# Kernel tuning notes

Hardware: AMD Instinct MI355X
Metric: run time of the kernel (lower is better)

## Reference

```python
import jax, jax.numpy as jnp
import numpy as np

SLEN, BSZ, D_MODEL, N_HEAD, D_HEAD, PROJ_DIM = 2048, 2, 1024, 16, 64, 256
LN_EPS = 1e-5
PRIME_EPS = 1e-4


def setup_inputs() -> dict:
    key = jax.random.key(0)
    ks = jax.random.split(key, 4)
    h = jax.random.normal(ks[0], (SLEN, BSZ, D_MODEL), jnp.float32)
    W_qkvb = jax.random.normal(ks[1], (D_MODEL, N_HEAD * (3 * D_HEAD + 1)), jnp.float32) * (D_MODEL ** -0.5)
    W_o = jax.random.normal(ks[2], (N_HEAD * D_HEAD, D_MODEL), jnp.float32) * ((N_HEAD * D_HEAD) ** -0.5)
    ln_gamma = jnp.ones((D_MODEL,), jnp.float32)
    ln_beta = jnp.zeros((D_MODEL,), jnp.float32)
    # orthogonal random matrix (d_head, proj_dim): blocks of orthonormal cols, rows scaled to norm sqrt(d)
    rng = np.random.default_rng(0)
    blocks = []
    for _ in range(PROJ_DIM // D_HEAD):
        qm, _ = np.linalg.qr(rng.standard_normal((D_HEAD, D_HEAD)))
        blocks.append(qm)
    pm = np.concatenate(blocks, axis=1) * np.sqrt(D_HEAD)
    proj_matrix = jnp.asarray(pm, jnp.float32)  # (d_head, proj_dim)
    return {"h": h, "W_qkvb": W_qkvb, "W_o": W_o, "ln_gamma": ln_gamma,
            "ln_beta": ln_beta, "proj_matrix": proj_matrix}


def prime(x, pm):
    # FAVOR+ hyperbolic softmax-kernel features. x: (B,H,L,d), pm: (d,m) -> (B,H,L,2m)
    d = x.shape[-1]
    m = pm.shape[-1]
    xn = x * (d ** -0.25)
    proj = jnp.einsum('bhld,dm->bhlm', xn, pm)
    hnorm = 0.5 * jnp.sum(xn * xn, axis=-1, keepdims=True)
    feat = jnp.concatenate([jnp.exp(proj - hnorm), jnp.exp(-proj - hnorm)], axis=-1)
    return ((2 * m) ** -0.5) * (feat + PRIME_EPS)


def layer_norm(x, gamma, beta):
    mu = jnp.mean(x, axis=-1, keepdims=True)
    var = jnp.mean(jnp.square(x - mu), axis=-1, keepdims=True)
    return (x - mu) * jax.lax.rsqrt(var + LN_EPS) * gamma + beta


def reference(h, W_qkvb, W_o, ln_gamma, ln_beta, proj_matrix):
    slen, bsz, _ = h.shape
    qkvb = (h @ W_qkvb).reshape(slen, bsz, N_HEAD, 3 * D_HEAD + 1)
    q, k, v, hb = jnp.split(qkvb, [D_HEAD, 2 * D_HEAD, 3 * D_HEAD], axis=-1)
    hb = jax.nn.sigmoid(hb)
    # (L,B,H,*) -> (B,H,L,*)
    q = q.transpose(1, 2, 0, 3)
    k = k.transpose(1, 2, 0, 3)
    v = v.transpose(1, 2, 0, 3)
    hb = hb.transpose(1, 2, 0, 3)
    qp = prime(q, proj_matrix)
    kp = prime(k, proj_matrix)
    kp = kp / kp.sum(-1, keepdims=True)
    qp = qp / qp.sum(-1, keepdims=True)
    # time-major for the scan: (L,B,H,*)
    qpT = qp.transpose(2, 0, 1, 3)
    kpT = kp.transpose(2, 0, 1, 3)
    vT = v.transpose(2, 0, 1, 3)
    hbT = hb.transpose(2, 0, 1, 3)
    W0 = jnp.zeros((bsz, N_HEAD, 2 * PROJ_DIM, D_HEAD), h.dtype)

    def step(W, inp):
        qt, kt, vt, bt = inp  # (B,H,2m),(B,H,2m),(B,H,d),(B,H,1)
        v_old = jnp.einsum('bhpd,bhp->bhd', W, kt)
        W = W + jnp.einsum('bhp,bhd->bhpd', kt, bt * (vt - v_old))
        out = jnp.einsum('bhpd,bhp->bhd', W, qt)
        return W, out

    _, outs = jax.lax.scan(step, W0, (qpT, kpT, vT, hbT))  # outs: (L,B,H,d)
    scale = D_HEAD ** -0.5
    layer_out = (scale * outs).reshape(slen, bsz, N_HEAD * D_HEAD)
    attn_out = layer_out @ W_o
    return layer_norm(h + attn_out, ln_gamma, ln_beta)
```

## Files before the change

### kernel.cpp

```cpp
#include <hip/hip_runtime.h>
#include <hip/hip_bf16.h>

#define LSEQ   2048
#define BSZN   2
#define DMODEL 1024
#define NHEAD  16
#define DH     64
#define MPROJ  256
#define PF     512
#define CHK    64
#define NCHK   32
#define BHN    32
#define NQKV   3088
#define NQPAD  3200

typedef __hip_bfloat16 bf16;
typedef short bf16x8 __attribute__((ext_vector_type(8)));
typedef float f32x4 __attribute__((ext_vector_type(4)));

#define MFMA(a, b, c) __builtin_amdgcn_mfma_f32_16x16x32_bf16(a, b, c, 0, 0, 0)

#define UNP(u, a, b) { a = __uint_as_float((unsigned)(u) << 16); b = __uint_as_float((unsigned)(u) & 0xffff0000u); }

static __device__ __forceinline__ float b2f(bf16 x) {
  unsigned short us = *(unsigned short*)&x;
  return __uint_as_float((unsigned)us << 16);
}
static __device__ __forceinline__ bf16 f2b(float x) { return __float2bfloat16(x); }
static __device__ __forceinline__ unsigned pkbf(float a, float b) {
  bf16 x = __float2bfloat16(a), y = __float2bfloat16(b);
  return ((unsigned)(*(unsigned short*)&y) << 16) | (unsigned)(*(unsigned short*)&x);
}

static __device__ __forceinline__ void gl_lds16(const void* gsrc, void* ldst) {
  __builtin_amdgcn_global_load_lds(
      (const __attribute__((address_space(1))) unsigned int*)gsrc,
      (__attribute__((address_space(3))) unsigned int*)ldst, 16, 0, 0);
}

#define MEMFENCE asm volatile("" ::: "memory")
#define WAITV(n) asm volatile("s_waitcnt vmcnt(" #n ")" ::: "memory")
#define WAITLGKM asm volatile("s_waitcnt lgkmcnt(0)" ::: "memory")
#define BARRIER() __builtin_amdgcn_s_barrier()

__global__ __launch_bounds__(256)
void k_cvth(const float* __restrict__ h, bf16* __restrict__ hbf)
{
  const int gt = blockIdx.x * 256 + threadIdx.x;
  const int r = gt >> 7, ug = gt & 127;
  const int grp = ug >> 3, u = ug & 7;
  const float4 f0 = *(const float4*)&h[(size_t)r * 1024 + grp * 64 + u * 8];
  const float4 f1 = *(const float4*)&h[(size_t)r * 1024 + grp * 64 + u * 8 + 4];
  uint4 o;
  o.x = pkbf(f0.x, f0.y); o.y = pkbf(f0.z, f0.w);
  o.z = pkbf(f1.x, f1.y); o.w = pkbf(f1.z, f1.w);
  *(uint4*)&hbf[(size_t)r * 1024 + grp * 64 + ((u ^ (r & 7)) << 3)] = o;
}

__global__ __launch_bounds__(256)
void k_cvtw(const float* __restrict__ W, bf16* __restrict__ WT, int nsrc)
{
  __shared__ float sT[64][65];
  const int tid = threadIdx.x;
  const int n0 = blockIdx.x * 64, k0 = blockIdx.y * 64;
#pragma unroll
  for (int j = 0; j < 16; j++) {
    const int e = j * 256 + tid;
    const int r = e >> 6, c = e & 63;
    sT[r][c] = (n0 + c < nsrc) ? W[(size_t)(k0 + r) * nsrc + n0 + c] : 0.f;
  }
  __syncthreads();
#pragma unroll
  for (int j = 0; j < 2; j++) {
    const int uid = j * 256 + tid;
    const int rp = uid >> 3, u = uid & 7;
    uint4 o;
    o.x = pkbf(sT[u * 8 + 0][rp], sT[u * 8 + 1][rp]);
    o.y = pkbf(sT[u * 8 + 2][rp], sT[u * 8 + 3][rp]);
    o.z = pkbf(sT[u * 8 + 4][rp], sT[u * 8 + 5][rp]);
    o.w = pkbf(sT[u * 8 + 6][rp], sT[u * 8 + 7][rp]);
    *(uint4*)&WT[(size_t)(n0 + rp) * 1024 + k0 + ((u ^ (rp & 7)) << 3)] = o;
  }
}

__global__ __launch_bounds__(256)
void k_cvtpm(const float* __restrict__ pm, bf16* __restrict__ pmThi,
             bf16* __restrict__ pmTlo)
{
  const int n = threadIdx.x;
  float v[64];
#pragma unroll
  for (int d = 0; d < 64; d++) v[d] = pm[d * MPROJ + n] * 0.35355339059327373f;
  const int key = n & 7;
#pragma unroll
  for (int u = 0; u < 8; u++) {
    unsigned hi[4], lo[4];
#pragma unroll
    for (int j = 0; j < 4; j++) {
      const float a = v[u * 8 + j * 2], b = v[u * 8 + j * 2 + 1];
      const bf16 ah = f2b(a), bh_ = f2b(b);
      const float ar = a - b2f(ah), br = b - b2f(bh_);
      hi[j] = ((unsigned)(*(const unsigned short*)&bh_) << 16) | (unsigned)(*(const unsigned short*)&ah);
      const bf16 al = f2b(ar), bl = f2b(br);
      lo[j] = ((unsigned)(*(const unsigned short*)&bl) << 16) | (unsigned)(*(const unsigned short*)&al);
    }
    *(uint4*)&pmThi[(size_t)n * 64 + ((u ^ key) << 3)] = make_uint4(hi[0], hi[1], hi[2], hi[3]);
    *(uint4*)&pmTlo[(size_t)n * 64 + ((u ^ key) << 3)] = make_uint4(lo[0], lo[1], lo[2], lo[3]);
  }
}

#define GEMM_STAGE(Abase, Bbase, kt, b) {                                      \
  const size_t kb = (size_t)(kt) * 128;           \
  _Pragma("unroll")                                                            \
  for (int j = 0; j < 4; j++) {                                                \
    const int row = (w * 4 + j) * 8 + (lane >> 3);                             \
    gl_lds16((const char*)(Abase) + (size_t)(m0 + row) * 2048 + kb + (lane & 7) * 16, \
             &sA[b][(w * 4 + j) * 1024]);                                      \
  }                                                                            \
  _Pragma("unroll")                                                            \
  for (int j = 0; j < 4; j++) {                                                \
    const int row = (w * 4 + j) * 8 + (lane >> 3);                             \
    gl_lds16((const char*)(Bbase) + (size_t)(n0 + row) * 2048 + kb + (lane & 7) * 16, \
             &sB[b][(w * 4 + j) * 1024]);                                      \
  } }

#define GEMM_COMPUTE(b) {                                                      \
  _Pragma("unroll")                                                            \
  for (int ks = 0; ks < 2; ks++) {                                             \
    bf16x8 af[4], bfr[4];                                                      \
    _Pragma("unroll")                                                          \
    for (int f = 0; f < 4; f++) {                                              \
      const int row = wm * 64 + f * 16 + l16;                                  \
      af[f] = *(const bf16x8*)&sA[b][row * 128 + (((ks * 4 + lg) ^ xs) << 4)]; \
    }                                                                          \
    _Pragma("unroll")                                                          \
    for (int f = 0; f < 4; f++) {                                              \
      const int row = wn * 64 + f * 16 + l16;                                  \
      bfr[f] = *(const bf16x8*)&sB[b][row * 128 + (((ks * 4 + lg) ^ xs) << 4)]; \
    }                                                                          \
    _Pragma("unroll")                                                          \
    for (int fm = 0; fm < 4; fm++)                                             \
      _Pragma("unroll")                                                        \
      for (int fn = 0; fn < 4; fn++)                                           \
        acc[fm][fn] = MFMA(af[fm], bfr[fn], acc[fm][fn]);                      \
  } }

#define GEMM_PREAMBLE                                                          \
  __shared__ __align__(16) char sA[2][16384];                                  \
  __shared__ __align__(16) char sB[2][16384];                                  \
  const int tid = threadIdx.x, w = tid >> 6, lane = tid & 63;                  \
  const int l16 = lane & 15, lg = lane >> 4;                                   \
  const int wm = w >> 1, wn = w & 1;                                           \
  const int m0 = blockIdx.y * 128, n0 = blockIdx.x * 128;                      \
  const int xs = l16 & 7;                                                      \
  f32x4 acc[4][4];                                                             \
  _Pragma("unroll")                                                            \
  for (int i = 0; i < 4; i++)                                                  \
    _Pragma("unroll")                                                          \
    for (int j = 0; j < 4; j++) acc[i][j] = (f32x4){0.f, 0.f, 0.f, 0.f};

__global__ __launch_bounds__(256, 2)
void k_gemm_qkvb(const bf16* __restrict__ A, const bf16* __restrict__ B,
                 bf16* __restrict__ qh, bf16* __restrict__ kh,
                 bf16* __restrict__ vh, float* __restrict__ bbuf)
{
  GEMM_PREAMBLE
  GEMM_STAGE(A, B, 0, 0);
  __syncthreads();
  for (int kt = 0; kt < 16; kt++) {
    const int b = kt & 1;
    if (kt < 15) GEMM_STAGE(A, B, kt + 1, b ^ 1);
    GEMM_COMPUTE(b);
    __syncthreads();
  }
#pragma unroll
  for (int fm = 0; fm < 4; fm++)
#pragma unroll
    for (int fn = 0; fn < 4; fn++)
#pragma unroll
      for (int reg = 0; reg < 4; reg++) {
        const int m = m0 + wm * 64 + fm * 16 + lg * 4 + reg;
        const int n = n0 + wn * 64 + fn * 16 + l16;
        if (n >= NQKV) continue;
        const float v = acc[fm][fn][reg];
        const int l = m >> 1, bidx = m & 1;
        const int hd = n / 193;
        const int rem = n - hd * 193;
        const int bhi = bidx * NHEAD + hd;
        const size_t o = ((size_t)bhi * LSEQ + l) * DH;
        if (rem < 64) {
          const int d = rem;
          qh[o + ((((d >> 3) ^ (l & 7)) << 3) | (d & 7))] = f2b(v);
        } else if (rem < 128) {
          const int d = rem - 64;
          kh[o + ((((d >> 3) ^ (l & 7)) << 3) | (d & 7))] = f2b(v);
        } else if (rem < 192) {
          vh[o + rem - 128] = f2b(v);
        } else {
          bbuf[(size_t)bhi * LSEQ + l] = 1.f / (1.f + __expf(-v));
        }
      }
}

__global__ __launch_bounds__(256, 2)
void k_gemm_out(const bf16* __restrict__ A, const bf16* __restrict__ B,
                const float* __restrict__ h, float* __restrict__ ao)
{
  GEMM_PREAMBLE
  GEMM_STAGE(A, B, 0, 0);
  __syncthreads();
  for (int kt = 0; kt < 16; kt++) {
    const int b = kt & 1;
    if (kt < 15) GEMM_STAGE(A, B, kt + 1, b ^ 1);
    GEMM_COMPUTE(b);
    __syncthreads();
  }
#pragma unroll
  for (int fm = 0; fm < 4; fm++)
#pragma unroll
    for (int fn = 0; fn < 4; fn++)
#pragma unroll
      for (int reg = 0; reg < 4; reg++) {
        const int m = m0 + wm * 64 + fm * 16 + lg * 4 + reg;
        const int n = n0 + wn * 64 + fn * 16 + l16;
        const size_t o = (size_t)m * DMODEL + n;
        ao[o] = acc[fm][fn][reg] + h[o];
      }
}

__global__ __launch_bounds__(256, 2)
void k_featm(const bf16* __restrict__ qh, const bf16* __restrict__ kh,
             const bf16* __restrict__ pmThi, const bf16* __restrict__ pmTlo,
             bf16* __restrict__ Qp, bf16* __restrict__ Kp)
{
  __shared__ __align__(16) char sPM[2][32768];
  __shared__ __align__(16) char sX[8192];

  const int tid = threadIdx.x, w = tid >> 6, lane = tid & 63;
  const int l16 = lane & 15, lg = lane >> 4;
  const int xs = l16 & 7;
  const int l0 = blockIdx.x * 64, bhi = blockIdx.y;

#pragma unroll
  for (int j = 0; j < 8; j++)
    gl_lds16((const char*)pmThi + (size_t)(w * 8 + j) * 1024 + lane * 16,
             &sPM[0][(w * 8 + j) * 1024]);
#pragma unroll
  for (int j = 0; j < 8; j++)
    gl_lds16((const char*)pmTlo + (size_t)(w * 8 + j) * 1024 + lane * 16,
             &sPM[1][(w * 8 + j) * 1024]);
  {
    const char* qb = (const char*)(qh + ((size_t)bhi * LSEQ + l0) * DH);
#pragma unroll
    for (int j = 0; j < 2; j++)
      gl_lds16(qb + (size_t)(w * 2 + j) * 1024 + lane * 16, &sX[(w * 2 + j) * 1024]);
  }
  MEMFENCE;
  WAITV(0); BARRIER();

  const int srow = w * 16 + l16;
  const size_t gsr = (size_t)bhi * LSEQ + l0 + srow;

  for (int wh = 0; wh < 2; wh++) {
    bf16* dst = wh ? Kp : Qp;

    float hn;
    {
      const char* xrow = &sX[srow * 128];
      const uint4 a0 = *(const uint4*)&xrow[lg * 32];
      const uint4 a1 = *(const uint4*)&xrow[lg * 32 + 16];
      float f0, f1, f2, f3, f4, f5, f6, f7, a = 0.f;
      UNP(a0.x, f0, f1); UNP(a0.y, f2, f3); UNP(a0.z, f4, f5); UNP(a0.w, f6, f7);
      a = fmaf(f0, f0, a); a = fmaf(f1, f1, a); a = fmaf(f2, f2, a); a = fmaf(f3, f3, a);
      a = fmaf(f4, f4, a); a = fmaf(f5, f5, a); a = fmaf(f6, f6, a); a = fmaf(f7, f7, a);
      UNP(a1.x, f0, f1); UNP(a1.y, f2, f3); UNP(a1.z, f4, f5); UNP(a1.w, f6, f7);
      a = fmaf(f0, f0, a); a = fmaf(f1, f1, a); a = fmaf(f2, f2, a); a = fmaf(f3, f3, a);
      a = fmaf(f4, f4, a); a = fmaf(f5, f5, a); a = fmaf(f6, f6, a); a = fmaf(f7, f7, a);
      a += __shfl_xor(a, 16); a += __shfl_xor(a, 32);
      hn = a * 0.0625f;
    }

    f32x4 acc[16];
#pragma unroll
    for (int i = 0; i < 16; i++) acc[i] = (f32x4){0.f, 0.f, 0.f, 0.f};
#pragma unroll
    for (int ks = 0; ks < 2; ks++) {
      const bf16x8 bx = *(const bf16x8*)&sX[srow * 128 + (((ks * 4 + lg) ^ xs) << 4)];
#pragma unroll
      for (int mt = 0; mt < 16; mt++) {
        const bf16x8 ah = *(const bf16x8*)&sPM[0][(mt * 16 + l16) * 128 + (((ks * 4 + lg) ^ xs) << 4)];
        acc[mt] = MFMA(ah, bx, acc[mt]);
        const bf16x8 al = *(const bf16x8*)&sPM[1][(mt * 16 + l16) * 128 + (((ks * 4 + lg) ^ xs) << 4)];
        acc[mt] = MFMA(al, bx, acc[mt]);
      }
    }

    if (wh == 0) {
      BARRIER();
      const char* kb = (const char*)(kh + ((size_t)bhi * LSEQ + l0) * DH);
#pragma unroll
      for (int j = 0; j < 2; j++)
        gl_lds16(kb + (size_t)(w * 2 + j) * 1024 + lane * 16, &sX[(w * 2 + j) * 1024]);
      MEMFENCE;
    }

    float ss = 0.f;
#pragma unroll
    for (int mt = 0; mt < 16; mt++)
#pragma unroll
      for (int r = 0; r < 4; r++) {
        const float p = acc[mt][r];
        ss += __expf(p - hn) + __expf(-p - hn);
      }
    ss += __shfl_xor(ss, 16); ss += __shfl_xor(ss, 32);
    const float D = ss + 0.0512f;
    const float cc = 1e-4f / D;
    const float eo = hn + __logf(D);

    const size_t gb = gsr * PF;
    const int half = (lg & 1) * 4;
    const int ub = lg >> 1;
#pragma unroll
    for (int mt = 0; mt < 16; mt++) {
      const float v0 = __expf(acc[mt][0] - eo) + cc;
      const float v1 = __expf(acc[mt][1] - eo) + cc;
      const float v2 = __expf(acc[mt][2] - eo) + cc;
      const float v3 = __expf(acc[mt][3] - eo) + cc;
      const float n0 = __expf(-acc[mt][0] - eo) + cc;
      const float n1 = __expf(-acc[mt][1] - eo) + cc;
      const float n2 = __expf(-acc[mt][2] - eo) + cc;
      const float n3 = __expf(-acc[mt][3] - eo) + cc;
      const int u = mt * 2 + ub;
      *(uint2*)&dst[gb + ((u ^ xs) << 3) + half] = make_uint2(pkbf(v0, v1), pkbf(v2, v3));
      *(uint2*)&dst[gb + (((u + 32) ^ xs) << 3) + half] = make_uint2(pkbf(n0, n1), pkbf(n2, n3));
      __builtin_amdgcn_sched_barrier(0);
    }

    if (wh == 0) { WAITV(32); BARRIER(); }
  }
}

__global__ __launch_bounds__(256, 2)
void k_sgsolve(const bf16* __restrict__ Kp, const bf16* __restrict__ Qp,
               const float* __restrict__ bbuf,
               bf16* __restrict__ Gl, bf16* __restrict__ Tm,
               bf16* __restrict__ KpT)
{
  __shared__ __align__(16) char bufK[2][8192];
  __shared__ __align__(16) char bufQ[2][8192];
  __shared__ float sS[CHK][65];
  __shared__ float sT[CHK][65];
  __shared__ float sBeta[CHK];

  const int tid = threadIdx.x, w = tid >> 6, lane = tid & 63;
  const int l16 = lane & 15, lg = lane >> 4;
  const int xs = l16 & 7;
  const int c = blockIdx.x, bhi = blockIdx.y;
  const size_t cb = ((size_t)bhi * LSEQ + (size_t)c * CHK) * PF;
  const size_t rowb = (size_t)bhi * LSEQ + (size_t)c * CHK;
  const size_t ktb = (((size_t)bhi * NCHK + c) * 512) * 64;
  const size_t sb = (((size_t)bhi * NCHK + c) * CHK) * CHK;

  if (tid < CHK) sBeta[tid] = bbuf[rowb + tid];

  f32x4 accS[4], accG[4];
#pragma unroll
  for (int i = 0; i < 4; i++) { accS[i] = (f32x4){0.f,0.f,0.f,0.f}; accG[i] = (f32x4){0.f,0.f,0.f,0.f}; }

#define SG_STAGE(win, b) {                                                     \
  _Pragma("unroll")                                                            \
  for (int j = 0; j < 2; j++) {                                                \
    const int row = w * 16 + j * 8 + (lane >> 3);                              \
    gl_lds16((const char*)(Kp + cb) + (size_t)row * 1024 + (size_t)(win) * 128 + (lane & 7) * 16, \
             &bufK[b][(w * 16 + j * 8) * 128]);                                \
  }                                                                            \
  _Pragma("unroll")                                                            \
  for (int j = 0; j < 2; j++) {                                                \
    const int row = w * 16 + j * 8 + (lane >> 3);                              \
    gl_lds16((const char*)(Qp + cb) + (size_t)row * 1024 + (size_t)(win) * 128 + (lane & 7) * 16, \
             &bufQ[b][(w * 16 + j * 8) * 128]);                                \
  } }

  SG_STAGE(0, 0);
  MEMFENCE;

  for (int win = 0; win < 8; win++) {
    const int b = win & 1;
    if (win < 7) { SG_STAGE(win + 1, b ^ 1); MEMFENCE; }
    if (win == 0)      { WAITV(4); }
    else if (win < 7)  { WAITV(6); }
    else               { WAITV(2); }
    BARRIER();

#pragma unroll
    for (int ks = 0; ks < 2; ks++) {
      const bf16x8 aK = *(const bf16x8*)&bufK[b][(16 * w + l16) * 128 + (((ks * 4 + lg) ^ xs) << 4)];
      const bf16x8 aQ = *(const bf16x8*)&bufQ[b][(16 * w + l16) * 128 + (((ks * 4 + lg) ^ xs) << 4)];
      bf16x8 bK[4];
#pragma unroll
      for (int nt = 0; nt < 4; nt++)
        bK[nt] = *(const bf16x8*)&bufK[b][(nt * 16 + l16) * 128 + (((ks * 4 + lg) ^ xs) << 4)];
#pragma unroll
      for (int nt = 0; nt < 4; nt++) {
        accS[nt] = MFMA(aK, bK[nt], accS[nt]);
        accG[nt] = MFMA(aQ, bK[nt], accG[nt]);
      }
    }

#pragma unroll
    for (int jj = 0; jj < 2; jj++) {
      const int idx = jj * 256 + tid;
      const int pl = idx >> 3, l8 = idx & 7;
      unsigned short v[8];
#pragma unroll
      for (int j = 0; j < 8; j++) {
        const int l = l8 * 8 + j;
        v[j] = *(const unsigned short*)&bufK[b][l * 128 + (((pl >> 3) ^ (l & 7)) << 4) + (pl & 7) * 2];
      }
      uint4 o;
      o.x = ((unsigned)v[1] << 16) | v[0];
      o.y = ((unsigned)v[3] << 16) | v[2];
      o.z = ((unsigned)v[5] << 16) | v[4];
      o.w = ((unsigned)v[7] << 16) | v[6];
      const int p = win * 64 + pl;
      *(uint4*)&KpT[ktb + (size_t)p * 64 + ((l8 ^ (p & 7)) << 3)] = o;
    }
    BARRIER();
  }
#undef SG_STAGE

#pragma unroll
  for (int nt = 0; nt < 4; nt++)
#pragma unroll
    for (int reg = 0; reg < 4; reg++) {
      const int ri = 16 * w + lg * 4 + reg;
      const int cj = nt * 16 + l16;
      sS[ri][cj] = accS[nt][reg];
      Gl[sb + ri * 64 + (((cj >> 3) ^ (ri & 7)) << 3) + (cj & 7)] =
          f2b((cj <= ri) ? accG[nt][reg] : 0.f);
    }
  __syncthreads();

  if (tid < CHK) {
    const int j = tid;
    for (int i = 0; i < CHK; i++) {
      float acc = (i == j) ? 1.f : 0.f;
      for (int k = 0; k < i; k++) acc = fmaf(-sS[i][k], sT[k][j], acc);
      sT[i][j] = sBeta[i] * acc;
    }
  }
  __syncthreads();
  for (int t = tid; t < CHK * CHK; t += 256) {
    const int r = t >> 6, ccj = t & 63;
    Tm[sb + r * 64 + (((ccj >> 3) ^ (r & 7)) << 3) + (ccj & 7)] = f2b(sT[r][ccj]);
  }
}

__global__ __launch_bounds__(512, 2)
void k_scan(const bf16* __restrict__ Kp, const bf16* __restrict__ Qp,
            const bf16* __restrict__ vh, const bf16* __restrict__ Tm,
            const bf16* __restrict__ Gl, const bf16* __restrict__ KpT,
            bf16* __restrict__ lobf)
{
  __shared__ __align__(16) char bufA[65536];
  __shared__ __align__(16) char bufB[65536];
  __shared__ __align__(16) char sWT[16384];
  __shared__ __align__(16) char suP[2048];
  __shared__ __align__(16) char sUT[2048];
  __shared__ __align__(16) float pbuf[4][16][16];

  const int tid = threadIdx.x;
  const int w = tid >> 6, lane = tid & 63;
  const int l16 = lane & 15, lg = lane >> 4;
  const int wp = w >> 1, h = w & 1;
  const int bhi = blockIdx.x & 31, dq = blockIdx.x >> 5;
  const int bidx = bhi >> 4, hd = bhi & 15;
  const int xs = l16 & 7;

  char* RA = bufA + w * 8192;
  char* RB = bufB + w * 8192;

  for (int i = tid; i < 4096; i += 512) ((unsigned*)sWT)[i] = 0u;

  f32x4 Wacc[4];
#pragma unroll
  for (int i = 0; i < 4; i++) Wacc[i] = (f32x4){0.f, 0.f, 0.f, 0.f};

  const size_t bh_base = (size_t)bhi * LSEQ * PF;
  const size_t tg0 = ((size_t)bhi * NCHK) * 4096;
  const size_t kt0 = ((size_t)bhi * NCHK) * (512 * 64);

  {
    const char* gt = (const char*)(KpT + kt0);
#pragma unroll
    for (int j = 0; j < 8; j++)
      gl_lds16(gt + (size_t)w * 8192 + j * 1024 + lane * 16, RB + j * 1024);
    const char* g = (const char*)(Kp + bh_base);
#pragma unroll
    for (int j = 0; j < 8; j++)
      gl_lds16(g + (size_t)(16 * wp + 2 * j + (lane >> 5)) * 1024 + h * 512 + (lane & 31) * 16,
               RA + j * 1024);
  }
  MEMFENCE;
  WAITV(0); WAITLGKM; BARRIER();

  for (int c = 0; c < NCHK; c++) {
    BARRIER();

    const size_t cb = bh_base + (size_t)c * CHK * PF;
    const bf16* TmC  = Tm + tg0 + (size_t)c * 4096;
    const bf16* GlC  = Gl + tg0 + (size_t)c * 4096;
    const char* QpC  = (const char*)(Qp + cb);
    const char* KpN  = (const char*)(Kp + cb + CHK * PF);
    const char* KpTN = (const char*)(KpT + kt0 + (size_t)(c + 1) * (512 * 64));
    const int trow = 16 * wp + l16;

    float v0 = 0.f, v1 = 0.f, v2 = 0.f, v3 = 0.f;
    bf16x8 tf0 = {}, tf1 = {}, gf0 = {}, gf1 = {};
    if (!h) {
      const bf16* vp = vh + ((size_t)bhi * LSEQ + c * 64 + wp * 16 + lg * 4) * 64 + dq * 16 + l16;
      v0 = b2f(vp[0]);   v1 = b2f(vp[64]);
      v2 = b2f(vp[128]); v3 = b2f(vp[192]);
      tf0 = *(const bf16x8*)&TmC[trow * 64 + ((lg ^ xs) << 3)];
      tf1 = *(const bf16x8*)&TmC[trow * 64 + (((4 + lg) ^ xs) << 3)];
      gf0 = *(const bf16x8*)&GlC[trow * 64 + ((lg ^ xs) << 3)];
      gf1 = *(const bf16x8*)&GlC[trow * 64 + (((4 + lg) ^ xs) << 3)];
    }
    MEMFENCE;
    if (!h) { WAITV(12); } else { WAITV(0); }

    f32x4 a0v = (f32x4){0.f,0.f,0.f,0.f}, a1v = (f32x4){0.f,0.f,0.f,0.f};
    bf16x8 wb[8];
#pragma unroll
    for (int ks = 0; ks < 8; ks += 2) {
      const bf16x8 aa0 = *(const bf16x8*)&RA[l16 * 512 + (((ks * 4 + lg) ^ xs) << 4)];
      wb[ks] = *(const bf16x8*)&sWT[l16 * 1024 + ((((h * 32 + ks * 4 + lg)) ^ xs) << 4)];
      a0v = MFMA(aa0, wb[ks], a0v);
      const bf16x8 aa1 = *(const bf16x8*)&RA[l16 * 512 + ((((ks + 1) * 4 + lg) ^ xs) << 4)];
      wb[ks + 1] = *(const bf16x8*)&sWT[l16 * 1024 + ((((h * 32 + (ks + 1) * 4 + lg)) ^ xs) << 4)];
      a1v = MFMA(aa1, wb[ks + 1], a1v);
    }
    if (h) {
      float4 pv;
      pv.x = a0v[0] + a1v[0]; pv.y = a0v[1] + a1v[1];
      pv.z = a0v[2] + a1v[2]; pv.w = a0v[3] + a1v[3];
      *(float4*)&pbuf[wp][l16][lg * 4] = pv;
    }
    WAITLGKM;
    BARRIER();

#pragma unroll
    for (int j = 0; j < 8; j++)
      gl_lds16(QpC + (size_t)(16 * wp + 2 * j + (lane >> 5)) * 1024 + h * 512 + (lane & 31) * 16,
               RA + j * 1024);
    MEMFENCE;

    if (!h) {
      WAITV(8);
      const float4 po = *(const float4*)&pbuf[wp][l16][lg * 4];
      const float u0 = v0 - (a0v[0] + a1v[0]) - po.x;
      const float u1 = v1 - (a0v[1] + a1v[1]) - po.y;
      const float u2 = v2 - (a0v[2] + a1v[2]) - po.z;
      const float u3 = v3 - (a0v[3] + a1v[3]) - po.w;
      const int l0r = 16 * wp + lg * 4;
      *(uint2*)&suP[l16 * 128 + (((l0r >> 3) ^ xs) << 4) + (l0r & 7) * 2] =
          make_uint2(pkbf(u0, u1), pkbf(u2, u3));
    }
    WAITLGKM;
    BARRIER();

    if (!h) {
      f32x4 ua = (f32x4){0.f,0.f,0.f,0.f};
      ua = MFMA(tf0, *(const bf16x8*)&suP[l16 * 128 + ((lg ^ xs) << 4)], ua);
      ua = MFMA(tf1, *(const bf16x8*)&suP[l16 * 128 + (((4 + lg) ^ xs) << 4)], ua);
      const int l0r = 16 * wp + lg * 4;
      *(uint2*)&sUT[l16 * 128 + (((l0r >> 3) ^ xs) << 4) + (l0r & 7) * 2] =
          make_uint2(pkbf(ua[0], ua[1]), pkbf(ua[2], ua[3]));
    }
    WAITLGKM;
    BARRIER();

    const bf16x8 bu0 = *(const bf16x8*)&sUT[l16 * 128 + ((lg ^ xs) << 4)];
    const bf16x8 bu1 = *(const bf16x8*)&sUT[l16 * 128 + (((4 + lg) ^ xs) << 4)];
#pragma unroll
    for (int mt = 0; mt < 4; mt++) {
      const int pr = mt * 16 + l16;
      const bf16x8 ka0 = *(const bf16x8*)&RB[pr * 128 + ((lg ^ xs) << 4)];
      Wacc[mt] = MFMA(ka0, bu0, Wacc[mt]);
      const bf16x8 ka1 = *(const bf16x8*)&RB[pr * 128 + (((4 + lg) ^ xs) << 4)];
      Wacc[mt] = MFMA(ka1, bu1, Wacc[mt]);
    }
    WAITLGKM;
    if (c < NCHK - 1) {
#pragma unroll
      for (int j = 0; j < 8; j++)
        gl_lds16(KpTN + (size_t)w * 8192 + j * 1024 + lane * 16, RB + j * 1024);
      MEMFENCE;
    }
#pragma unroll
    for (int mt = 0; mt < 4; mt++) {
      const int p0m = w * 64 + mt * 16 + lg * 4;
      *(uint2*)&sWT[l16 * 1024 + (((p0m >> 3) ^ xs) << 4) + (p0m & 7) * 2] =
          make_uint2(pkbf(Wacc[mt][0], Wacc[mt][1]), pkbf(Wacc[mt][2], Wacc[mt][3]));
    }

    if (c < NCHK - 1) { WAITV(8); } else { WAITV(0); }
    f32x4 o0 = (f32x4){0.f,0.f,0.f,0.f}, o1 = (f32x4){0.f,0.f,0.f,0.f};
#pragma unroll
    for (int ks = 0; ks < 8; ks += 2) {
      const bf16x8 qa0 = *(const bf16x8*)&RA[l16 * 512 + (((ks * 4 + lg) ^ xs) << 4)];
      o0 = MFMA(qa0, wb[ks], o0);
      const bf16x8 qa1 = *(const bf16x8*)&RA[l16 * 512 + ((((ks + 1) * 4 + lg) ^ xs) << 4)];
      o1 = MFMA(qa1, wb[ks + 1], o1);
    }
    WAITLGKM;
    if (c < NCHK - 1) {
#pragma unroll
      for (int j = 0; j < 8; j++)
        gl_lds16(KpN + (size_t)(16 * wp + 2 * j + (lane >> 5)) * 1024 + h * 512 + (lane & 31) * 16,
                 RA + j * 1024);
      MEMFENCE;
    }
    if (h) {
      float4 pv;
      pv.x = o0[0] + o1[0]; pv.y = o0[1] + o1[1];
      pv.z = o0[2] + o1[2]; pv.w = o0[3] + o1[3];
      *(float4*)&pbuf[wp][l16][lg * 4] = pv;
    } else {
      o0 = MFMA(gf0, bu0, o0);
      o1 = MFMA(gf1, bu1, o1);
    }
    WAITLGKM;
    BARRIER();

    if (!h) {
      const float4 po = *(const float4*)&pbuf[wp][l16][lg * 4];
      const float pr4[4] = {po.x, po.y, po.z, po.w};
      const int colb = hd * 64 + dq * 16 + l16;
#pragma unroll
      for (int reg = 0; reg < 4; reg++) {
        const int l = c * 64 + 16 * wp + lg * 4 + reg;
        const int r = l * BSZN + bidx;
        const int cp = (colb & ~63) | ((((colb >> 3) & 7) ^ (r & 7)) << 3) | (colb & 7);
        lobf[(size_t)r * DMODEL + cp] = f2b(0.125f * (o0[reg] + o1[reg] + pr4[reg]));
      }
    }
    WAITLGKM;
  }
}

__global__ __launch_bounds__(256)
void k_ln(const float* __restrict__ ao, const float* __restrict__ gamma,
          const float* __restrict__ beta, float* __restrict__ out)
{
  const int row = blockIdx.x;
  const int tid = threadIdx.x;
  __shared__ float r1[4], r2[4];
  const float4 v = *(const float4*)&ao[(size_t)row * DMODEL + tid * 4];
  float s1 = v.x + v.y + v.z + v.w;
  float s2 = v.x * v.x + v.y * v.y + v.z * v.z + v.w * v.w;
  for (int off = 32; off > 0; off >>= 1) {
    s1 += __shfl_down(s1, off);
    s2 += __shfl_down(s2, off);
  }
  if ((tid & 63) == 0) { r1[tid >> 6] = s1; r2[tid >> 6] = s2; }
  __syncthreads();
  const float ts1 = r1[0] + r1[1] + r1[2] + r1[3];
  const float ts2 = r2[0] + r2[1] + r2[2] + r2[3];
  const float mu = ts1 * (1.f / DMODEL);
  const float var = ts2 * (1.f / DMODEL) - mu * mu;
  const float rs = rsqrtf(var + 1e-5f);
  const float4 g = *(const float4*)&gamma[tid * 4];
  const float4 b = *(const float4*)&beta[tid * 4];
  float4 o;
  o.x = (v.x - mu) * rs * g.x + b.x;
  o.y = (v.y - mu) * rs * g.y + b.y;
  o.z = (v.z - mu) * rs * g.z + b.z;
  o.w = (v.w - mu) * rs * g.w + b.w;
  *(float4*)&out[(size_t)row * DMODEL + tid * 4] = o;
}

extern "C" void kernel_launch(void* const* d_in, const int* in_sizes, int n_in,
                              void* d_out, int out_size, void* d_ws, size_t ws_size,
                              hipStream_t stream)
{
  (void)in_sizes; (void)n_in; (void)out_size; (void)ws_size;
  const float* h   = (const float*)d_in[0];
  const float* Wq  = (const float*)d_in[1];
  const float* Wo  = (const float*)d_in[2];
  const float* gam = (const float*)d_in[3];
  const float* bet = (const float*)d_in[4];
  const float* pm  = (const float*)d_in[5];
  float* out = (float*)d_out;

  char* ws = (char*)d_ws;
  size_t off = 0;
  auto alloc = [&](size_t bytes) -> void* {
    void* p = ws + off;
    off += (bytes + 255) & ~(size_t)255;
    return p;
  };
  bf16*  vh  = (bf16*)alloc((size_t)BHN * LSEQ * DH * 2);
  float* bbf = (float*)alloc((size_t)BHN * LSEQ * 4);
  bf16*  Kp  = (bf16*)alloc((size_t)BHN * LSEQ * PF * 2);
  bf16*  Qp  = (bf16*)alloc((size_t)BHN * LSEQ * PF * 2);
  bf16*  Tm  = (bf16*)alloc((size_t)BHN * NCHK * CHK * CHK * 2);
  bf16*  Gll = (bf16*)alloc((size_t)BHN * NCHK * CHK * CHK * 2);
  char*  R   = (char*)alloc((size_t)BHN * NCHK * 512 * 64 * 2);
  bf16*  WoT = (bf16*)alloc((size_t)DMODEL * DMODEL * 2);
  bf16*  pmThi = (bf16*)alloc((size_t)MPROJ * 64 * 2);
  bf16*  pmTlo = (bf16*)alloc((size_t)MPROJ * 64 * 2);
  bf16*  qh  = (bf16*)R;
  bf16*  kh  = (bf16*)(R + (size_t)BHN * LSEQ * DH * 2);
  bf16*  hbf = (bf16*)(R + (size_t)2 * BHN * LSEQ * DH * 2);
  bf16*  WqT = (bf16*)(R + (size_t)3 * BHN * LSEQ * DH * 2);
  bf16*  KpT = (bf16*)R;
  float* ao  = (float*)R;
  bf16*  lobf = (bf16*)d_out;

  k_cvth     <<<dim3(2048),                       256, 0, stream>>>(h, hbf);
  k_cvtw     <<<dim3(NQPAD / 64, 16),             256, 0, stream>>>(Wq, WqT, NQKV);
  k_cvtw     <<<dim3(DMODEL / 64, 16),            256, 0, stream>>>(Wo, WoT, DMODEL);
  k_cvtpm    <<<dim3(1),                          256, 0, stream>>>(pm, pmThi, pmTlo);
  k_gemm_qkvb<<<dim3(NQPAD / 128, 4096 / 128),    256, 0, stream>>>(hbf, WqT, qh, kh, vh, bbf);
  k_featm    <<<dim3(LSEQ / 64, BHN),             256, 0, stream>>>(qh, kh, pmThi, pmTlo, Qp, Kp);
  k_sgsolve  <<<dim3(NCHK, BHN),                  256, 0, stream>>>(Kp, Qp, bbf, Gll, Tm, KpT);
  k_scan     <<<dim3(128),                        512, 0, stream>>>(Kp, Qp, vh, Tm, Gll, KpT, lobf);
  k_gemm_out <<<dim3(DMODEL / 128, 4096 / 128),   256, 0, stream>>>(lobf, WoT, h, ao);
  k_ln       <<<dim3(4096),                       256, 0, stream>>>(ao, gam, bet, out);
}
```

Before: 367.9 us.

## Load scan operands directly into registers instead of staging through LDS

The chunked delta-rule scan kernel stops staging Kp, Qp and KpT tiles through 128KB of shared memory with global-to-LDS copies. Each wave now loads its MFMA fragments straight from global memory into registers and prefetches the next chunk's fragments after the current ones are consumed. The T/G/v loads for the next chunk are also hoisted to the end of the previous iteration. This cuts LDS usage, which could allow more blocks per CU, and removes LDS round trips. In exchange it raises register pressure under launch bounds of 512 threads, and the global reads are less coalesced.

```diff
diff --git a/kernel.cpp b/kernel.cpp
--- a/kernel.cpp
+++ b/kernel.cpp
@@ -462,8 +462,6 @@
             const bf16* __restrict__ Gl, const bf16* __restrict__ KpT,
             bf16* __restrict__ lobf)
 {
-  __shared__ __align__(16) char bufA[65536];
-  __shared__ __align__(16) char bufB[65536];
   __shared__ __align__(16) char sWT[16384];
   __shared__ __align__(16) char suP[2048];
   __shared__ __align__(16) char sUT[2048];
@@ -476,9 +474,7 @@
   const int bhi = blockIdx.x & 31, dq = blockIdx.x >> 5;
   const int bidx = bhi >> 4, hd = bhi & 15;
   const int xs = l16 & 7;
-
-  char* RA = bufA + w * 8192;
-  char* RB = bufB + w * 8192;
+  const int trow = 16 * wp + l16;
 
   for (int i = tid; i < 4096; i += 512) ((unsigned*)sWT)[i] = 0u;
 
@@ -490,73 +486,63 @@
   const size_t tg0 = ((size_t)bhi * NCHK) * 4096;
   const size_t kt0 = ((size_t)bhi * NCHK) * (512 * 64);
 
-  {
-    const char* gt = (const char*)(KpT + kt0);
-#pragma unroll
-    for (int j = 0; j < 8; j++)
-      gl_lds16(gt + (size_t)w * 8192 + j * 1024 + lane * 16, RB + j * 1024);
-    const char* g = (const char*)(Kp + bh_base);
-#pragma unroll
-    for (int j = 0; j < 8; j++)
-      gl_lds16(g + (size_t)(16 * wp + 2 * j + (lane >> 5)) * 1024 + h * 512 + (lane & 31) * 16,
-               RA + j * 1024);
-  }
-  MEMFENCE;
-  WAITV(0); WAITLGKM; BARRIER();
+  const bf16* KpF = Kp + bh_base + (size_t)trow * PF + h * 256;
+  const bf16* QpF = Qp + bh_base + (size_t)trow * PF + h * 256;
+  const bf16* KTF = KpT + kt0 + (size_t)(64 * w + l16) * 64;
+
+  bf16x8 fKp[8], fQp[8], fKT[8];
+  bf16x8 tf0 = {}, tf1 = {}, gf0 = {}, gf1 = {};
+  float v0 = 0.f, v1 = 0.f, v2 = 0.f, v3 = 0.f;
+
+#define LOADKP(c) { const bf16* _b = KpF + (size_t)(c) * CHK * PF;             \
+  _Pragma("unroll")                                                            \
+  for (int ks = 0; ks < 8; ks++)                                               \
+    fKp[ks] = *(const bf16x8*)(_b + (((ks * 4 + lg) ^ xs) << 3)); }
+#define LOADQP(c) { const bf16* _b = QpF + (size_t)(c) * CHK * PF;             \
+  _Pragma("unroll")                                                            \
+  for (int ks = 0; ks < 8; ks++)                                               \
+    fQp[ks] = *(const bf16x8*)(_b + (((ks * 4 + lg) ^ xs) << 3)); }
+#define LOADKT(c) { const bf16* _b = KTF + (size_t)(c) * (512 * 64);           \
+  _Pragma("unroll")                                                            \
+  for (int mt = 0; mt < 4; mt++) {                                             \
+    fKT[mt * 2]     = *(const bf16x8*)(_b + mt * 16 * 64 + (((    lg) ^ xs) << 3)); \
+    fKT[mt * 2 + 1] = *(const bf16x8*)(_b + mt * 16 * 64 + (((4 + lg) ^ xs) << 3)); \
+  } }
+#define LOADTG(c) if (!h) {                                                    \
+  const bf16* _t = Tm + tg0 + (size_t)(c) * 4096;                              \
+  const bf16* _g = Gl + tg0 + (size_t)(c) * 4096;                              \
+  tf0 = *(const bf16x8*)&_t[trow * 64 + ((lg ^ xs) << 3)];                     \
+  tf1 = *(const bf16x8*)&_t[trow * 64 + (((4 + lg) ^ xs) << 3)];               \
+  gf0 = *(const bf16x8*)&_g[trow * 64 + ((lg ^ xs) << 3)];                     \
+  gf1 = *(const bf16x8*)&_g[trow * 64 + (((4 + lg) ^ xs) << 3)];               \
+  const bf16* _v = vh + ((size_t)bhi * LSEQ + (c) * 64 + wp * 16 + lg * 4) * 64 + dq * 16 + l16; \
+  v0 = b2f(_v[0]); v1 = b2f(_v[64]); v2 = b2f(_v[128]); v3 = b2f(_v[192]); }
+
+  LOADKP(0); LOADKT(0); LOADQP(0); LOADTG(0);
+  WAITLGKM; BARRIER();
 
   for (int c = 0; c < NCHK; c++) {
     BARRIER();
 
-    const size_t cb = bh_base + (size_t)c * CHK * PF;
-    const bf16* TmC  = Tm + tg0 + (size_t)c * 4096;
-    const bf16* GlC  = Gl + tg0 + (size_t)c * 4096;
-    const char* QpC  = (const char*)(Qp + cb);
-    const char* KpN  = (const char*)(Kp + cb + CHK * PF);
-    const char* KpTN = (const char*)(KpT + kt0 + (size_t)(c + 1) * (512 * 64));
-    const int trow = 16 * wp + l16;
-
-    float v0 = 0.f, v1 = 0.f, v2 = 0.f, v3 = 0.f;
-    bf16x8 tf0 = {}, tf1 = {}, gf0 = {}, gf1 = {};
-    if (!h) {
-      const bf16* vp = vh + ((size_t)bhi * LSEQ + c * 64 + wp * 16 + lg * 4) * 64 + dq * 16 + l16;
-      v0 = b2f(vp[0]);   v1 = b2f(vp[64]);
-      v2 = b2f(vp[128]); v3 = b2f(vp[192]);
-      tf0 = *(const bf16x8*)&TmC[trow * 64 + ((lg ^ xs) << 3)];
-      tf1 = *(const bf16x8*)&TmC[trow * 64 + (((4 + lg) ^ xs) << 3)];
-      gf0 = *(const bf16x8*)&GlC[trow * 64 + ((lg ^ xs) << 3)];
-      gf1 = *(const bf16x8*)&GlC[trow * 64 + (((4 + lg) ^ xs) << 3)];
-    }
-    MEMFENCE;
-    if (!h) { WAITV(12); } else { WAITV(0); }
-
     f32x4 a0v = (f32x4){0.f,0.f,0.f,0.f}, a1v = (f32x4){0.f,0.f,0.f,0.f};
     bf16x8 wb[8];
 #pragma unroll
     for (int ks = 0; ks < 8; ks += 2) {
-      const bf16x8 aa0 = *(const bf16x8*)&RA[l16 * 512 + (((ks * 4 + lg) ^ xs) << 4)];
-      wb[ks] = *(const bf16x8*)&sWT[l16 * 1024 + ((((h * 32 + ks * 4 + lg)) ^ xs) << 4)];
-      a0v = MFMA(aa0, wb[ks], a0v);
-      const bf16x8 aa1 = *(const bf16x8*)&RA[l16 * 512 + ((((ks + 1) * 4 + lg) ^ xs) << 4)];
-      wb[ks + 1] = *(const bf16x8*)&sWT[l16 * 1024 + ((((h * 32 + (ks + 1) * 4 + lg)) ^ xs) << 4)];
-      a1v = MFMA(aa1, wb[ks + 1], a1v);
-    }
+      wb[ks] = *(const bf16x8*)&sWT[l16 * 1024 + (((h * 32 + ks * 4 + lg) ^ xs) << 4)];
+      a0v = MFMA(fKp[ks], wb[ks], a0v);
+      wb[ks + 1] = *(const bf16x8*)&sWT[l16 * 1024 + (((h * 32 + (ks + 1) * 4 + lg) ^ xs) << 4)];
+      a1v = MFMA(fKp[ks + 1], wb[ks + 1], a1v);
+    }
+    if (c < NCHK - 1) LOADKP(c + 1);
     if (h) {
       float4 pv;
       pv.x = a0v[0] + a1v[0]; pv.y = a0v[1] + a1v[1];
       pv.z = a0v[2] + a1v[2]; pv.w = a0v[3] + a1v[3];
       *(float4*)&pbuf[wp][l16][lg * 4] = pv;
     }
-    WAITLGKM;
-    BARRIER();
-
-#pragma unroll
-    for (int j = 0; j < 8; j++)
-      gl_lds16(QpC + (size_t)(16 * wp + 2 * j + (lane >> 5)) * 1024 + h * 512 + (lane & 31) * 16,
-               RA + j * 1024);
-    MEMFENCE;
+    WAITLGKM; BARRIER();
 
     if (!h) {
-      WAITV(8);
       const float4 po = *(const float4*)&pbuf[wp][l16][lg * 4];
       const float u0 = v0 - (a0v[0] + a1v[0]) - po.x;
       const float u1 = v1 - (a0v[1] + a1v[1]) - po.y;
@@ -566,8 +552,7 @@
       *(uint2*)&suP[l16 * 128 + (((l0r >> 3) ^ xs) << 4) + (l0r & 7) * 2] =
           make_uint2(pkbf(u0, u1), pkbf(u2, u3));
     }
-    WAITLGKM;
-    BARRIER();
+    WAITLGKM; BARRIER();
 
     if (!h) {
       f32x4 ua = (f32x4){0.f,0.f,0.f,0.f};
@@ -577,26 +562,16 @@
       *(uint2*)&sUT[l16 * 128 + (((l0r >> 3) ^ xs) << 4) + (l0r & 7) * 2] =
           make_uint2(pkbf(ua[0], ua[1]), pkbf(ua[2], ua[3]));
     }
-    WAITLGKM;
-    BARRIER();
+    WAITLGKM; BARRIER();
 
     const bf16x8 bu0 = *(const bf16x8*)&sUT[l16 * 128 + ((lg ^ xs) << 4)];
     const bf16x8 bu1 = *(const bf16x8*)&sUT[l16 * 128 + (((4 + lg) ^ xs) << 4)];
 #pragma unroll
     for (int mt = 0; mt < 4; mt++) {
-      const int pr = mt * 16 + l16;
-      const bf16x8 ka0 = *(const bf16x8*)&RB[pr * 128 + ((lg ^ xs) << 4)];
-      Wacc[mt] = MFMA(ka0, bu0, Wacc[mt]);
-      const bf16x8 ka1 = *(const bf16x8*)&RB[pr * 128 + (((4 + lg) ^ xs) << 4)];
-      Wacc[mt] = MFMA(ka1, bu1, Wacc[mt]);
-    }
-    WAITLGKM;
-    if (c < NCHK - 1) {
-#pragma unroll
-      for (int j = 0; j < 8; j++)
-        gl_lds16(KpTN + (size_t)w * 8192 + j * 1024 + lane * 16, RB + j * 1024);
-      MEMFENCE;
-    }
+      Wacc[mt] = MFMA(fKT[mt * 2], bu0, Wacc[mt]);
+      Wacc[mt] = MFMA(fKT[mt * 2 + 1], bu1, Wacc[mt]);
+    }
+    if (c < NCHK - 1) LOADKT(c + 1);
 #pragma unroll
     for (int mt = 0; mt < 4; mt++) {
       const int p0m = w * 64 + mt * 16 + lg * 4;
@@ -604,23 +579,13 @@
           make_uint2(pkbf(Wacc[mt][0], Wacc[mt][1]), pkbf(Wacc[mt][2], Wacc[mt][3]));
     }
 
-    if (c < NCHK - 1) { WAITV(8); } else { WAITV(0); }
     f32x4 o0 = (f32x4){0.f,0.f,0.f,0.f}, o1 = (f32x4){0.f,0.f,0.f,0.f};
 #pragma unroll
     for (int ks = 0; ks < 8; ks += 2) {
-      const bf16x8 qa0 = *(const bf16x8*)&RA[l16 * 512 + (((ks * 4 + lg) ^ xs) << 4)];
-      o0 = MFMA(qa0, wb[ks], o0);
-      const bf16x8 qa1 = *(const bf16x8*)&RA[l16 * 512 + ((((ks + 1) * 4 + lg) ^ xs) << 4)];
-      o1 = MFMA(qa1, wb[ks + 1], o1);
-    }
-    WAITLGKM;
-    if (c < NCHK - 1) {
-#pragma unroll
-      for (int j = 0; j < 8; j++)
-        gl_lds16(KpN + (size_t)(16 * wp + 2 * j + (lane >> 5)) * 1024 + h * 512 + (lane & 31) * 16,
-                 RA + j * 1024);
-      MEMFENCE;
-    }
+      o0 = MFMA(fQp[ks], wb[ks], o0);
+      o1 = MFMA(fQp[ks + 1], wb[ks + 1], o1);
+    }
+    if (c < NCHK - 1) LOADQP(c + 1);
     if (h) {
       float4 pv;
       pv.x = o0[0] + o1[0]; pv.y = o0[1] + o1[1];
@@ -630,8 +595,7 @@
       o0 = MFMA(gf0, bu0, o0);
       o1 = MFMA(gf1, bu1, o1);
     }
-    WAITLGKM;
-    BARRIER();
+    WAITLGKM; BARRIER();
 
     if (!h) {
       const float4 po = *(const float4*)&pbuf[wp][l16][lg * 4];
@@ -645,8 +609,13 @@
         lobf[(size_t)r * DMODEL + cp] = f2b(0.125f * (o0[reg] + o1[reg] + pr4[reg]));
       }
     }
+    if (c < NCHK - 1) LOADTG(c + 1);
     WAITLGKM;
   }
+#undef LOADKP
+#undef LOADQP
+#undef LOADKT
+#undef LOADTG
 }
 
 __global__ __launch_bounds__(256)
```

New measurement: 379.5 us. 1.03x slower.
